# Kernel tuning notes

Measured on AMD Instinct MI355X. Metric: run time of the kernel, lower is better.

Reference implementation:

```python
import jax, jax.numpy as jnp
import numpy as np

B, T, C, H = 4, 2048, 1024, 16
HD = C // H
SCALE = 1.0 / np.sqrt(HD).astype(np.float32)


def setup_inputs() -> dict:
    key = jax.random.key(0)
    k1, k2, k3, k4 = jax.random.split(key, 4)
    x = jax.random.normal(k1, (B, T, C), dtype=jnp.float32)
    keys = jax.random.normal(k2, (B, T, C), dtype=jnp.float32)
    queries = jax.random.normal(k3, (B, T, C), dtype=jnp.float32)
    mask = jnp.ones((B, T), dtype=jnp.float32)
    Wp = jax.random.normal(k4, (C, C), dtype=jnp.float32) * (1.0 / np.sqrt(C))
    bp = jnp.zeros((C,), dtype=jnp.float32)
    return {"x": x, "keys": keys, "queries": queries, "mask": mask, "Wp": Wp, "bp": bp}


def reference(x, keys, queries, mask, Wp, bp):
    Bc, Tc, Cc = x.shape
    # [B,T,C] -> [B,H,T,hd]
    def split_heads(t):
        return t.reshape(Bc, Tc, H, HD).transpose(0, 2, 1, 3)

    m = mask[:, None, :, None]  # [B,1,T,1]
    q = split_heads(queries) * m
    k = split_heads(keys) * m
    v = split_heads(x) * m
    # no softmax: linear bilinear attention; dropout=0 (eval) is identity
    att = jnp.einsum('bhqd,bhkd->bhqk', q, k) * SCALE  # [B,H,T,T]
    y = jnp.einsum('bhqk,bhkd->bhqd', att, v)          # [B,H,T,hd]
    y = y.transpose(0, 2, 1, 3).reshape(Bc, Tc, Cc)
    y = y @ Wp.T + bp  # torch Linear: x W^T + b
    return (y, att)
```

## Files before the change

kernel.cpp:

```cpp
#include <hip/hip_runtime.h>

#define Bdim 4
#define T 2048
#define C 1024
#define H 16
#define HD 64
#define SCALE 0.125f

typedef __attribute__((ext_vector_type(8))) short short8;
typedef __attribute__((ext_vector_type(4))) float f32x4;

__device__ inline unsigned short f2bf(float f) {
  unsigned int u = __float_as_uint(f);
  return (unsigned short)((u + 0x7FFFu + ((u >> 16) & 1u)) >> 16);
}

#define OFF_QS   (0u)
#define OFF_KS   (16u*1024u*1024u)
#define OFF_PART (32u*1024u*1024u)
#define OFF_GT   (32u*1024u*1024u)
#define OFF_KTV  (48u*1024u*1024u)

__global__ __launch_bounds__(256) void k_convert_qk(
    const float* __restrict__ queries, const float* __restrict__ keys,
    const float* __restrict__ mask,
    unsigned short* __restrict__ Qs, unsigned short* __restrict__ Ks) {
  int idx = blockIdx.x * 256 + threadIdx.x;
  long e = (long)idx * 8;
  int b = (int)(e / ((long)T * C));
  int rem = (int)(e % ((long)T * C));
  int t = rem / C;
  int c = rem % C;
  int h = c >> 6, d = c & 63;
  float m = mask[b * T + t];
  const float4* qp = (const float4*)(queries + e);
  const float4* kp = (const float4*)(keys + e);
  float4 q0 = qp[0], q1 = qp[1];
  float4 k0 = kp[0], k1 = kp[1];
  float qv[8] = {q0.x,q0.y,q0.z,q0.w,q1.x,q1.y,q1.z,q1.w};
  float kv[8] = {k0.x,k0.y,k0.z,k0.w,k1.x,k1.y,k1.z,k1.w};
  unsigned short qo[8], ko[8];
  #pragma unroll
  for (int j = 0; j < 8; ++j) {
    qo[j] = f2bf(qv[j] * m * SCALE);
    ko[j] = f2bf(kv[j] * m);
  }
  long dst = ((long)(b * H + h) * T + t) * HD + d;
  *(short8*)(Qs + dst) = *(const short8*)qo;
  *(short8*)(Ks + dst) = *(const short8*)ko;
}

__global__ __launch_bounds__(256) void k_att(
    const unsigned short* __restrict__ Qs, const unsigned short* __restrict__ Ks,
    float* __restrict__ att) {
  int bid = blockIdx.x;
  int wg = ((bid & 7) << 11) | (bid >> 3);
  int bh = wg >> 8;
  int tile = wg & 255;
  int tm = tile >> 4, tn = tile & 15;
  int tid = threadIdx.x;
  int lane = tid & 63, wid = tid >> 6;
  int wr = wid >> 1, wc = wid & 1;
  int lr = lane & 15, kg = lane >> 4;
  const unsigned short* Q = Qs + (long)bh * T * HD;
  const unsigned short* K = Ks + (long)bh * T * HD;
  int row0 = tm * 128 + wr * 64;
  int col0 = tn * 128 + wc * 64;
  short8 a[4][2], b[4][2];
  #pragma unroll
  for (int i = 0; i < 4; ++i) {
    #pragma unroll
    for (int kk = 0; kk < 2; ++kk) {
      a[i][kk] = *(const short8*)(Q + (long)(row0 + i*16 + lr)*HD + kk*32 + kg*8);
      b[i][kk] = *(const short8*)(K + (long)(col0 + i*16 + lr)*HD + kk*32 + kg*8);
    }
  }
  float* ob = att + (long)bh * T * T;
  #pragma unroll
  for (int i = 0; i < 4; ++i) {
    long rbase = (long)(row0 + i*16 + lr) * T + col0 + kg*4;
    #pragma unroll
    for (int j = 0; j < 4; ++j) {
      f32x4 acc = (f32x4){0.f, 0.f, 0.f, 0.f};
      acc = __builtin_amdgcn_mfma_f32_16x16x32_bf16(b[j][0], a[i][0], acc, 0, 0, 0);
      acc = __builtin_amdgcn_mfma_f32_16x16x32_bf16(b[j][1], a[i][1], acc, 0, 0, 0);
      *(f32x4*)(ob + rbase + j*16) = acc;
    }
  }
}

__global__ __launch_bounds__(256) void k_ktv_partial(
    const float* __restrict__ keys, const float* __restrict__ x,
    const float* __restrict__ mask, float* __restrict__ part) {
  int bid = blockIdx.x;
  int bh = bid >> 4, p = bid & 15;
  int b = bh >> 4, h = bh & 15;
  __shared__ float ks[16][64];
  __shared__ float vs[16][64];
  int tid = threadIdx.x;
  int ty = tid >> 4, tx = tid & 15;
  float acc[4][4];
  #pragma unroll
  for (int i = 0; i < 4; ++i)
    #pragma unroll
    for (int j = 0; j < 4; ++j) acc[i][j] = 0.f;
  int tbeg = p * 128;
  for (int t0 = tbeg; t0 < tbeg + 128; t0 += 16) {
    __syncthreads();
    for (int e = tid; e < 1024; e += 256) {
      int tt = e >> 6, d = e & 63;
      long gi = ((long)(b * T + t0 + tt)) * C + h * 64 + d;
      float m = mask[b * T + t0 + tt];
      ks[tt][d] = keys[gi] * m;
      vs[tt][d] = x[gi] * m;
    }
    __syncthreads();
    #pragma unroll 4
    for (int tt = 0; tt < 16; ++tt) {
      float ka[4], va[4];
      #pragma unroll
      for (int i = 0; i < 4; ++i) { ka[i] = ks[tt][ty + 16*i]; va[i] = vs[tt][tx + 16*i]; }
      #pragma unroll
      for (int i = 0; i < 4; ++i)
        #pragma unroll
        for (int j = 0; j < 4; ++j) acc[i][j] += ka[i] * va[j];
    }
  }
  float* o = part + (long)bid * 4096;
  #pragma unroll
  for (int i = 0; i < 4; ++i)
    #pragma unroll
    for (int j = 0; j < 4; ++j) o[(ty + 16*i) * 64 + tx + 16*j] = acc[i][j];
}

__global__ __launch_bounds__(256) void k_ktv_reduce(
    const float* __restrict__ part, float* __restrict__ ktv) {
  int i = blockIdx.x * 256 + threadIdx.x;
  int bh = i >> 12, off = i & 4095;
  const float* pp = part + ((long)bh << 16) + off;
  float s = 0.f;
  #pragma unroll
  for (int p = 0; p < 16; ++p) s += pp[p * 4096];
  ktv[i] = s;
}

__global__ __launch_bounds__(256) void k_gt(
    const float* __restrict__ ktv, const float* __restrict__ Wp,
    unsigned short* __restrict__ Gt) {
  int bid = blockIdx.x;
  int b = bid >> 8;
  int h = (bid >> 4) & 15;
  int n0 = (bid & 15) * 64;
  __shared__ float kv[64][64];
  __shared__ float wp[64][65];
  int tid = threadIdx.x;
  for (int e = tid; e < 4096; e += 256) {
    kv[e >> 6][e & 63] = ktv[((b * H + h) << 12) + e];
    wp[e >> 6][e & 63] = Wp[(long)(n0 + (e >> 6)) * C + h * 64 + (e & 63)];
  }
  __syncthreads();
  int nl = tid & 63, dg = tid >> 6;
  float s[16];
  #pragma unroll
  for (int dd = 0; dd < 16; ++dd) s[dd] = 0.f;
  for (int e = 0; e < 64; ++e) {
    float w = wp[nl][e];
    #pragma unroll
    for (int dd = 0; dd < 16; ++dd)
      s[dd] += kv[dg * 16 + dd][e] * w;
  }
  unsigned short o[16];
  #pragma unroll
  for (int dd = 0; dd < 16; ++dd) o[dd] = f2bf(s[dd]);
  unsigned short* dst = Gt + ((long)(b * C + n0 + nl)) * C + h * 64 + dg * 16;
  *(short8*)dst = *(const short8*)o;
  *(short8*)(dst + 8) = *(const short8*)(o + 8);
}

__global__ __launch_bounds__(256) void k_out(
    const unsigned short* __restrict__ Qs, const unsigned short* __restrict__ Gt,
    const float* __restrict__ bp, float* __restrict__ y) {
  int bid = blockIdx.x;
  int wg = ((bid & 7) << 6) | (bid >> 3);
  int b = wg >> 7;
  int tile = wg & 127;
  int tm = tile >> 3, tn = tile & 7;
  int tid = threadIdx.x;
  int lane = tid & 63, wid = tid >> 6;
  int wr = wid >> 1, wc = wid & 1;
  int lr = lane & 15, kg = lane >> 4;
  int row0 = tm * 128 + wr * 64;
  int col0 = tn * 128 + wc * 64;
  f32x4 acc[4][4];
  #pragma unroll
  for (int i = 0; i < 4; ++i)
    #pragma unroll
    for (int j = 0; j < 4; ++j) acc[i][j] = (f32x4){0.f, 0.f, 0.f, 0.f};
  #pragma unroll 4
  for (int k0 = 0; k0 < C; k0 += 32) {
    int h = k0 >> 6;
    int off = (k0 & 63) + kg * 8;
    const unsigned short* qb = Qs + (long)(b * H + h) * T * HD;
    const unsigned short* gb = Gt + (long)b * C * C + k0 + kg * 8;
    short8 av[4], bv[4];
    #pragma unroll
    for (int i = 0; i < 4; ++i)
      av[i] = *(const short8*)(qb + (long)(row0 + i*16 + lr) * HD + off);
    #pragma unroll
    for (int j = 0; j < 4; ++j)
      bv[j] = *(const short8*)(gb + (long)(col0 + j*16 + lr) * C);
    #pragma unroll
    for (int i = 0; i < 4; ++i)
      #pragma unroll
      for (int j = 0; j < 4; ++j)
        acc[i][j] = __builtin_amdgcn_mfma_f32_16x16x32_bf16(bv[j], av[i], acc[i][j], 0, 0, 0);
  }
  #pragma unroll
  for (int i = 0; i < 4; ++i) {
    int row = row0 + i*16 + lr;
    float* yrow = y + (long)(b * T + row) * C;
    #pragma unroll
    for (int j = 0; j < 4; ++j) {
      int col = col0 + j*16 + kg*4;
      f32x4 res = acc[i][j] + *(const f32x4*)(bp + col);
      *(f32x4*)(yrow + col) = res;
    }
  }
}

extern "C" void kernel_launch(void* const* d_in, const int* in_sizes, int n_in,
                              void* d_out, int out_size, void* d_ws, size_t ws_size,
                              hipStream_t stream) {
  const float* x       = (const float*)d_in[0];
  const float* keys    = (const float*)d_in[1];
  const float* queries = (const float*)d_in[2];
  const float* mask    = (const float*)d_in[3];
  const float* Wp      = (const float*)d_in[4];
  const float* bp      = (const float*)d_in[5];

  float* y   = (float*)d_out;
  float* att = (float*)d_out + (long)Bdim * T * C;

  char* ws = (char*)d_ws;
  unsigned short* Qs   = (unsigned short*)(ws + OFF_QS);
  unsigned short* Ks   = (unsigned short*)(ws + OFF_KS);
  float* part          = (float*)(ws + OFF_PART);
  float* ktv           = (float*)(ws + OFF_KTV);
  unsigned short* Gt   = (unsigned short*)(ws + OFF_GT);

  k_convert_qk<<<dim3(4096), dim3(256), 0, stream>>>(queries, keys, mask, Qs, Ks);
  k_ktv_partial<<<dim3(1024), dim3(256), 0, stream>>>(keys, x, mask, part);
  k_att<<<dim3(16384), dim3(256), 0, stream>>>(Qs, Ks, att);
  k_ktv_reduce<<<dim3(1024), dim3(256), 0, stream>>>(part, ktv);
  k_gt<<<dim3(1024), dim3(256), 0, stream>>>(ktv, Wp, Gt);
  k_out<<<dim3(512), dim3(256), 0, stream>>>(Qs, Gt, bp, y);
}
```

Measured before the change: 420.5 us.

## Retile attention-score kernel into full-row strips of 32 query rows

The att kernel now gives each workgroup 32 query rows and the full 2048-column span, with each wave sweeping 512 columns in 16-wide steps. The old version used 128x128 tiles. This cuts the grid from 16384 to 4096 blocks and makes each block write whole contiguous row segments of the large fp32 att output, aiming for better write streaming and less launch overhead. The cost is that K fragments are loaded from global memory inside the loop and reused across only two query sub-tiles, so there is less register-level reuse per load.

```diff
diff --git a/kernel.cpp b/kernel.cpp
--- a/kernel.cpp
+++ b/kernel.cpp
@@ -54,37 +54,34 @@
     const unsigned short* __restrict__ Qs, const unsigned short* __restrict__ Ks,
     float* __restrict__ att) {
   int bid = blockIdx.x;
-  int wg = ((bid & 7) << 11) | (bid >> 3);
-  int bh = wg >> 8;
-  int tile = wg & 255;
-  int tm = tile >> 4, tn = tile & 15;
+  int wg = ((bid & 7) << 9) | (bid >> 3);
+  int bh = wg >> 6;
+  int t0 = (wg & 63) * 32;
   int tid = threadIdx.x;
   int lane = tid & 63, wid = tid >> 6;
-  int wr = wid >> 1, wc = wid & 1;
   int lr = lane & 15, kg = lane >> 4;
   const unsigned short* Q = Qs + (long)bh * T * HD;
   const unsigned short* K = Ks + (long)bh * T * HD;
-  int row0 = tm * 128 + wr * 64;
-  int col0 = tn * 128 + wc * 64;
-  short8 a[4][2], b[4][2];
-  #pragma unroll
-  for (int i = 0; i < 4; ++i) {
-    #pragma unroll
-    for (int kk = 0; kk < 2; ++kk) {
-      a[i][kk] = *(const short8*)(Q + (long)(row0 + i*16 + lr)*HD + kk*32 + kg*8);
-      b[i][kk] = *(const short8*)(K + (long)(col0 + i*16 + lr)*HD + kk*32 + kg*8);
-    }
-  }
-  float* ob = att + (long)bh * T * T;
-  #pragma unroll
-  for (int i = 0; i < 4; ++i) {
-    long rbase = (long)(row0 + i*16 + lr) * T + col0 + kg*4;
-    #pragma unroll
-    for (int j = 0; j < 4; ++j) {
+  short8 a[2][2];
+  #pragma unroll
+  for (int i = 0; i < 2; ++i)
+    #pragma unroll
+    for (int kk = 0; kk < 2; ++kk)
+      a[i][kk] = *(const short8*)(Q + (long)(t0 + i*16 + lr)*HD + kk*32 + kg*8);
+  int colw = wid * 512;
+  float* ob = att + (long)bh * T * T + (long)t0 * T;
+  #pragma unroll 2
+  for (int j = 0; j < 32; ++j) {
+    int col = colw + j * 16;
+    const unsigned short* kp = K + (long)(col + lr) * HD + kg * 8;
+    short8 b0 = *(const short8*)(kp);
+    short8 b1 = *(const short8*)(kp + 32);
+    #pragma unroll
+    for (int i = 0; i < 2; ++i) {
       f32x4 acc = (f32x4){0.f, 0.f, 0.f, 0.f};
-      acc = __builtin_amdgcn_mfma_f32_16x16x32_bf16(b[j][0], a[i][0], acc, 0, 0, 0);
-      acc = __builtin_amdgcn_mfma_f32_16x16x32_bf16(b[j][1], a[i][1], acc, 0, 0, 0);
-      *(f32x4*)(ob + rbase + j*16) = acc;
+      acc = __builtin_amdgcn_mfma_f32_16x16x32_bf16(b0, a[i][0], acc, 0, 0, 0);
+      acc = __builtin_amdgcn_mfma_f32_16x16x32_bf16(b1, a[i][1], acc, 0, 0, 0);
+      *(f32x4*)(ob + (long)(i*16 + lr) * T + col + kg*4) = acc;
     }
   }
 }
@@ -250,7 +247,7 @@
 
   k_convert_qk<<<dim3(4096), dim3(256), 0, stream>>>(queries, keys, mask, Qs, Ks);
   k_ktv_partial<<<dim3(1024), dim3(256), 0, stream>>>(keys, x, mask, part);
-  k_att<<<dim3(16384), dim3(256), 0, stream>>>(Qs, Ks, att);
+  k_att<<<dim3(4096), dim3(256), 0, stream>>>(Qs, Ks, att);
   k_ktv_reduce<<<dim3(1024), dim3(256), 0, stream>>>(part, ktv);
   k_gt<<<dim3(1024), dim3(256), 0, stream>>>(ktv, Wp, Gt);
   k_out<<<dim3(512), dim3(256), 0, stream>>>(Qs, Gt, bp, y);
```

After: 485.9 us. 1.16x slower.
